# Performance work log

Measured on AMD Instinct MI355X. Metric: run time of the kernel, lower is better.

## Reference

```python
import jax, jax.numpy as jnp
import numpy as np

B, S, D, K = 16, 1024, 512, 4
DIL = (1, 2, 4, 8)
EPS_BN = 1e-5
EPS_LN = 1e-5


def _edge_conv1d(x, w, b, dilation):
    # x: [B, C, S], w: [O, C, k]; replicate ('edge') padding keeps length S
    p = (w.shape[-1] - 1) * dilation // 2
    xp = jnp.pad(x, ((0, 0), (0, 0), (p, p)), mode='edge')
    y = jax.lax.conv_general_dilated(xp, w, (1,), 'VALID', rhs_dilation=(dilation,),
                                     dimension_numbers=('NCH', 'OIH', 'NCH'))
    return y + b[None, :, None]


def setup_inputs() -> dict:
    key = jax.random.key(0)
    ks = jax.random.split(key, 16)
    g = lambda i, shape, s: jax.random.normal(ks[i], shape, jnp.float32) * s
    return {
        'x': g(0, (B, S, D), 1.0),
        'conv_w': g(1, (4, D, D, 3), 0.02),
        'conv_b': jnp.zeros((4, D), jnp.float32),
        'fusion_w': g(2, (D, 4 * D), 0.02),
        'fusion_b': jnp.zeros((D,), jnp.float32),
        'refine_w': g(3, (D, D, 3), 0.02),
        'refine_b': jnp.zeros((D,), jnp.float32),
        'hyp1_w': g(4, (D, D, 3), 0.02),
        'hyp1_b': jnp.zeros((D,), jnp.float32),
        'bn_gamma': jnp.ones((D,), jnp.float32),
        'bn_beta': jnp.zeros((D,), jnp.float32),
        'hyp2_w': g(5, (D // 2, D, 3), 0.02),
        'hyp2_b': jnp.zeros((D // 2,), jnp.float32),
        'proj_w': g(6, (2 * K, D // 2), 0.05),
        'proj_b': jnp.zeros((2 * K,), jnp.float32),
        'gate_w': g(7, (D, D), 0.02),
        'gate_b': jnp.zeros((D,), jnp.float32),
        'base_w': g(8, (D, D), 0.02),
        'base_b': jnp.zeros((D,), jnp.float32),
        'wav_w': g(9, (K, D, D), 0.02),
        'wav_b': jnp.zeros((K, D), jnp.float32),
        'ln_gamma': jnp.ones((D,), jnp.float32),
        'ln_beta': jnp.zeros((D,), jnp.float32),
    }


def _forward(x, conv_w, conv_b, fusion_w, fusion_b, refine_w, refine_b,
             hyp1_w, hyp1_b, bn_gamma, bn_beta, hyp2_w, hyp2_b,
             proj_w, proj_b, gate_w, gate_b, base_w, base_b,
             wav_w, wav_b, ln_gamma, ln_beta):
    residual = x
    x_in = jnp.transpose(x, (0, 2, 1))                      # [B, D, S]
    # ---- FFT trend/seasonal split ----
    fx = jnp.fft.rfft(x_in, axis=2)
    cutoff = S // 10
    mask = (jnp.arange(fx.shape[2]) < cutoff).astype(fx.dtype)
    x_seasonal = jnp.fft.irfft(fx * mask, n=S, axis=2)       # [B, D, S]
    x_smooth = x_seasonal
    x_spike = x_in - x_seasonal
    # ---- iterative dilated-conv smoothing (dropout = identity, eval mode) ----
    for _ in range(2):  # iterations
        outs = [jax.nn.gelu(_edge_conv1d(x_smooth, conv_w[i], conv_b[i], DIL[i]),
                            approximate=False)
                for i in range(4)]
        x_concat = jnp.concatenate(outs, axis=1)             # [B, 4D, S]
        x_smooth = jnp.einsum('oc,bcs->bos', fusion_w, x_concat) + fusion_b[None, :, None]
        x_spike = _edge_conv1d(x_in - x_smooth, refine_w, refine_b, 1)
    x_smooth_t = jnp.transpose(x_smooth, (0, 2, 1))          # [B, S, D]
    x_spike_t = jnp.transpose(x_spike, (0, 2, 1))            # [B, S, D]
    # ---- hypernet (BatchNorm in eval mode: running mean 0, var 1) ----
    h = _edge_conv1d(x_smooth, hyp1_w, hyp1_b, 1)
    h = h / jnp.sqrt(1.0 + EPS_BN) * bn_gamma[None, :, None] + bn_beta[None, :, None]
    h = jax.nn.silu(h)
    h = jax.nn.silu(_edge_conv1d(h, hyp2_w, hyp2_b, 1))      # [B, D/2, S]
    cnn_feat = jnp.mean(h, axis=2)                           # AdaptiveAvgPool1d(1)
    params = (cnn_feat @ proj_w.T + proj_b).reshape(B, 1, K, 2)
    dyn_a = jax.nn.softplus(params[..., 0]) + 0.01           # [B, 1, K]
    dyn_b = jax.nn.sigmoid(params[..., 1]) * S               # [B, 1, K]
    # ---- wavelet-KAN base path: Linear(silu(x_smooth)) ----
    base_out = jnp.einsum('bsd,ed->bse', jax.nn.silu(x_smooth_t), base_w) + base_b
    # ---- wavelet path: mexican-hat wavelets over sequence positions ----
    pos = jnp.arange(S, dtype=x.dtype)[None, :, None]        # [1, S, 1]
    u = (pos - dyn_b) / dyn_a                                # [B, S, K]
    c = 2.0 / (np.sqrt(3.0) * np.pi ** 0.25)
    psi = c * (1.0 - u * u) * jnp.exp(-0.5 * u * u)          # [B, S, K]
    z = jnp.einsum('bsd,kde->bkse', x_spike_t, wav_w)        # per-wavelet linear
    kan_out = jnp.einsum('bsk,bkse->bse', psi, z) + jnp.einsum('bsk,ke->bse', psi, wav_b)
    amp = jax.nn.sigmoid(base_out @ gate_w.T + gate_b) * 2.0
    x_out = base_out + kan_out * amp
    # ---- residual + LayerNorm ----
    y = x_out + residual
    mu = jnp.mean(y, axis=-1, keepdims=True)
    var = jnp.var(y, axis=-1, keepdims=True)
    return (y - mu) / jnp.sqrt(var + EPS_LN) * ln_gamma + ln_beta


def reference(x, conv_w, conv_b, fusion_w, fusion_b, refine_w, refine_b,
              hyp1_w, hyp1_b, bn_gamma, bn_beta, hyp2_w, hyp2_b,
              proj_w, proj_b, gate_w, gate_b, base_w, base_b,
              wav_w, wav_b, ln_gamma, ln_beta):
    return _forward(x, conv_w, conv_b, fusion_w, fusion_b, refine_w, refine_b,
                    hyp1_w, hyp1_b, bn_gamma, bn_beta, hyp2_w, hyp2_b,
                    proj_w, proj_b, gate_w, gate_b, base_w, base_b,
                    wav_w, wav_b, ln_gamma, ln_beta)
```

## Files before the change

kernel.cpp:

```cpp
#include <hip/hip_runtime.h>
#include <hip/hip_bf16.h>
#include <math.h>

#define NB 16
#define SS 1024
#define DD 512
#define SP 1040
#define HD 256

typedef unsigned short US;
typedef short bf16x8 __attribute__((ext_vector_type(8)));
typedef float f32x4 __attribute__((ext_vector_type(4)));
typedef __attribute__((address_space(1))) const void gv1;
typedef __attribute__((address_space(3))) void lv3;

static __device__ __forceinline__ float b2sf(US u){ return __uint_as_float(((unsigned)u)<<16); }
static __device__ __forceinline__ US f2b(float f){
  __hip_bfloat16 h = __float2bfloat16(f);
  union { __hip_bfloat16 h; US u; } c; c.h = h; return c.u;
}
static __device__ __forceinline__ float rd(const void* __restrict__ p, long i, int isf){
  return isf ? ((const float*)p)[i] : b2sf(((const US*)p)[i]);
}

__global__ void k_detect(const void* __restrict__ x, int* __restrict__ flag){
  const US* u = (const US*)x;
  int t = threadIdx.x;
  float m = 0.f;
  for (int i = t; i < 4096; i += 256){
    float v = fabsf(b2sf(u[i]));
    if (isnan(v) || isinf(v)) v = 1e30f;
    m = fmaxf(m, v);
  }
  for (int off = 32; off; off >>= 1) m = fmaxf(m, __shfl_down(m, off));
  __shared__ float sh[4];
  if ((t & 63) == 0) sh[t >> 6] = m;
  __syncthreads();
  if (t == 0){
    float mm = fmaxf(fmaxf(sh[0], sh[1]), fmaxf(sh[2], sh[3]));
    flag[0] = (mm > 1e6f) ? 1 : 0;
  }
}

__global__ void k_cvt_f(const void* __restrict__ s, float* __restrict__ d, long n, const int* __restrict__ fl){
  int isf = fl[0];
  long i = (long)blockIdx.x*256 + threadIdx.x;
  if (i < n) d[i] = rd(s, i, isf);
}
__global__ void k_cvt_b(const void* __restrict__ s, US* __restrict__ d, long n, const int* __restrict__ fl){
  int isf = fl[0];
  long i = (long)blockIdx.x*256 + threadIdx.x;
  if (i < n) d[i] = f2b(rd(s, i, isf));
}
__global__ void k_repack3(const void* __restrict__ src, US* __restrict__ dst, int O, int C, const int* __restrict__ fl){
  int isf = fl[0];
  long i = (long)blockIdx.x*256 + threadIdx.x;
  long n = (long)O*3*C;
  if (i >= n) return;
  int o = (int)(i / (3*C)); int r = (int)(i - (long)o*3*C); int t = r / C; int c = r - t*C;
  dst[i] = f2b(rd(src, ((long)o*C + c)*3 + t, isf));
}
__global__ void k_repack_wav(const void* __restrict__ src, US* __restrict__ dst, const int* __restrict__ fl){
  int isf = fl[0];
  long i = (long)blockIdx.x*256 + threadIdx.x;
  if (i >= 4L*DD*DD) return;
  int k = (int)(i >> 18); long r = i & ((1<<18)-1); int e = (int)(r >> 9); int d = (int)(r & 511);
  dst[i] = f2b(rd(src, ((long)(k*DD + d))*DD + e, isf));
}
__global__ void k_build_g(float* __restrict__ g){
  int d = blockIdx.x*256 + threadIdx.x;
  if (d >= SS) return;
  float s = 1.f;
  for (int k = 1; k < 102; ++k){
    int r = (k*d) & (SS-1);
    s += 2.f * cosf(6.28318530718f * (float)r * (1.f/SS));
  }
  g[d] = s * (1.f/SS);
}
__global__ void k_build_cmat(const float* __restrict__ g, US* __restrict__ cm){
  int i = blockIdx.x*256 + threadIdx.x;
  if (i >= SS*SS) return;
  int t = i >> 10, s = i & (SS-1);
  cm[i] = f2b(g[(s - t) & (SS-1)]);
}
__global__ __launch_bounds__(256) void k_transpose_b(const void* __restrict__ x, US* __restrict__ xt, const int* __restrict__ fl){
  int isf = fl[0];
  __shared__ float tl[32][33];
  int b = blockIdx.z, s0 = blockIdx.x*32, d0 = blockIdx.y*32;
  int tx = threadIdx.x & 31, ty = threadIdx.x >> 5;
  for (int i = ty; i < 32; i += 8)
    tl[i][tx] = rd(x, ((long)(b*SS + s0+i))*DD + d0+tx, isf);
  __syncthreads();
  for (int i = ty; i < 32; i += 8)
    xt[((long)(b*DD + d0+i))*SS + s0+tx] = f2b(tl[tx][i]);
}
__global__ void k_pad_b(const US* __restrict__ src, const void* __restrict__ xsub, US* __restrict__ dst, const int* __restrict__ fl){
  long i = (long)blockIdx.x*256 + threadIdx.x;
  const long TOT = (long)NB*SP*128;
  if (i >= TOT) return;
  int c4 = (int)(i & 127);
  int j  = (int)((i >> 7) % SP);
  int b  = (int)(i / (128L*SP));
  int sr = j - 8; sr = sr < 0 ? 0 : (sr > SS-1 ? SS-1 : sr);
  long si = ((long)(b*SS + sr))*DD + c4*4;
  ushort4 sv = *(const ushort4*)&src[si];
  float v0=b2sf(sv.x), v1=b2sf(sv.y), v2=b2sf(sv.z), v3=b2sf(sv.w);
  if (xsub){
    if (fl[0]){
      float4 xv = *(const float4*)((const float*)xsub + si);
      v0 = xv.x - v0; v1 = xv.y - v1; v2 = xv.z - v2; v3 = xv.w - v3;
    } else {
      ushort4 xv = *(const ushort4*)((const US*)xsub + si);
      v0 = b2sf(xv.x) - v0; v1 = b2sf(xv.y) - v1; v2 = b2sf(xv.z) - v2; v3 = b2sf(xv.w) - v3;
    }
  }
  ushort4 o; o.x=f2b(v0); o.y=f2b(v1); o.z=f2b(v2); o.w=f2b(v3);
  *(ushort4*)&dst[((long)(b*SP + j))*DD + c4*4] = o;
}
__global__ void k_silu_b(const US* __restrict__ s, US* __restrict__ d){
  long i = (long)blockIdx.x*256 + threadIdx.x;
  if (i >= (long)NB*SS*DD/4) return;
  ushort4 sv = *(const ushort4*)&s[i*4];
  float v[4] = {b2sf(sv.x), b2sf(sv.y), b2sf(sv.z), b2sf(sv.w)};
  ushort4 o;
  US* op = (US*)&o;
  #pragma unroll
  for (int r = 0; r < 4; r++){ float t = v[r]; op[r] = f2b(t/(1.f + expf(-t))); }
  *(ushort4*)&d[i*4] = o;
}

template<int EPI, bool TAPPED>
__global__ __launch_bounds__(256) void k_mfma(
    const US* __restrict__ A, const US* __restrict__ Bact, void* __restrict__ Out,
    int NYB, int K, long sBbytes, int ldbB, int dil,
    long sOut, int ldo, int moff,
    const float* __restrict__ bias, const float* __restrict__ s1v, const float* __restrict__ s2v)
{
  __shared__ alignas(16) US As[128*64];
  __shared__ alignas(16) US Bs[128*64];
  const int bx = blockIdx.x;
  const int ny = bx % NYB;
  const int b  = bx / NYB;
  const int m0 = blockIdx.y*128, n0 = ny*128;
  const int dd = (TAPPED && dil < 0) ? (1 << (m0 >> 9)) : dil;
  const char* Bb = (const char*)Bact + (long)b*sBbytes;
  const int tid = threadIdx.x;
  const int lane = tid & 63, w = tid >> 6;
  const int wr = w >> 1, wc = w & 1;
  const int col = lane & 15, g = lane >> 4;

  f32x4 acc[4][4] = {};

  int rows_[4], sls_[4];
  #pragma unroll
  for (int i = 0; i < 4; i++){
    int c = w*256 + i*64 + lane;
    rows_[i] = c >> 3;
    sls_[i] = (c & 7) ^ ((c >> 3) & 7);
  }

  for (int k0 = 0; k0 < K; k0 += 64){
    const int c0 = TAPPED ? (k0 & 511) : k0;
    const int srowOff = TAPPED ? (8 + ((k0 >> 9) - 1)*dd) : 0;
    __syncthreads();
    #pragma unroll
    for (int i = 0; i < 4; i++){
      const char* ga = (const char*)A + ((long)(m0 + rows_[i])*K + k0)*2 + sls_[i]*16;
      __builtin_amdgcn_global_load_lds((gv1*)ga, (lv3*)&As[(w*256 + i*64)*8], 16, 0, 0);
      const char* gb = Bb + (long)(n0 + rows_[i] + srowOff)*ldbB + c0*2 + sls_[i]*16;
      __builtin_amdgcn_global_load_lds((gv1*)gb, (lv3*)&Bs[(w*256 + i*64)*8], 16, 0, 0);
    }
    __syncthreads();
    #pragma unroll
    for (int kk = 0; kk < 2; kk++){
      bf16x8 af[4], bf[4];
      #pragma unroll
      for (int f = 0; f < 4; f++){
        int rowa = wr*64 + f*16 + col;
        int sla = (g + kk*4) ^ (rowa & 7);
        af[f] = *(const bf16x8*)&As[rowa*64 + sla*8];
        int rowb = wc*64 + f*16 + col;
        int slb = (g + kk*4) ^ (rowb & 7);
        bf[f] = *(const bf16x8*)&Bs[rowb*64 + slb*8];
      }
      #pragma unroll
      for (int fm = 0; fm < 4; fm++)
        #pragma unroll
        for (int fn = 0; fn < 4; fn++)
          acc[fm][fn] = __builtin_amdgcn_mfma_f32_16x16x32_bf16(af[fm], bf[fn], acc[fm][fn], 0, 0, 0);
    }
  }

  #pragma unroll
  for (int fm = 0; fm < 4; fm++){
    const int mm = m0 + wr*64 + fm*16 + g*4;
    #pragma unroll
    for (int fn = 0; fn < 4; fn++){
      const int nn = n0 + wc*64 + fn*16 + col;
      f32x4 v = acc[fm][fn];
      if (EPI == 5){
        US* o = (US*)Out + (long)b*sOut + (long)mm*ldo + nn;
        #pragma unroll
        for (int r = 0; r < 4; r++) o[(long)r*ldo] = f2b(v[r]);
      } else {
        US pk[4];
        #pragma unroll
        for (int r = 0; r < 4; r++){
          int m = mm + r;
          float val = v[r] + bias[m];
          if (EPI == 1) val = 0.5f*val*(1.f + erff(val*0.70710678f));
          if (EPI == 2){ val = val*(s1v[m]*0.99999500f) + s2v[m]; val = val/(1.f + expf(-val)); }
          if (EPI == 3){ val = val/(1.f + expf(-val)); }
          pk[r] = f2b(val);
        }
        US* o = (US*)Out + (long)b*sOut + (long)nn*ldo + moff + mm;
        *(ushort4*)o = *(ushort4*)pk;
      }
    }
  }
}

__global__ __launch_bounds__(256) void k_pool(const US* __restrict__ h2, float* __restrict__ feat){
  int b = blockIdx.x, c = threadIdx.x;
  float s = 0.f;
  for (int t = 0; t < SS; t++) s += b2sf(h2[((long)(b*SS + t))*HD + c]);
  feat[b*HD + c] = s * (1.f/SS);
}
__global__ void k_params(const float* __restrict__ feat, const float* __restrict__ pw,
                         const float* __restrict__ pb, float* __restrict__ dynA, float* __restrict__ dynB){
  int t = threadIdx.x;
  if (t >= 128) return;
  int b = t >> 3, j = t & 7;
  float s = pb[j];
  for (int c = 0; c < HD; c++) s += feat[b*HD + c]*pw[j*HD + c];
  int k = j >> 1;
  if ((j & 1) == 0){
    float sp = s > 20.f ? s : log1pf(expf(s));
    dynA[b*4 + k] = sp + 0.01f;
  } else {
    dynB[b*4 + k] = 1024.f/(1.f + expf(-s));
  }
}
__global__ void k_psi(const float* __restrict__ dynA, const float* __restrict__ dynB, float* __restrict__ psi){
  int i = blockIdx.x*256 + threadIdx.x;
  if (i >= NB*4*SS) return;
  int b = i >> 12, k = (i >> 10) & 3, s = i & (SS-1);
  float u = ((float)s - dynB[b*4 + k]) / dynA[b*4 + k];
  psi[i] = 0.86732507f*(1.f - u*u)*expf(-0.5f*u*u);
}
__global__ __launch_bounds__(128) void k_final(const US* __restrict__ base, const US* __restrict__ zz,
    const US* __restrict__ gate, const float* __restrict__ psi, const void* __restrict__ x,
    void* __restrict__ out, const float* __restrict__ lng, const float* __restrict__ lnb,
    const int* __restrict__ fl){
  int isf = fl[0];
  long row = blockIdx.x;
  int b = (int)(row >> 10), s = (int)(row & (SS-1));
  int t = threadIdx.x;
  long off = row*DD + t*4;
  ushort4 bs = *(const ushort4*)&base[off];
  ushort4 gt = *(const ushort4*)&gate[off];
  float p0 = psi[b*4096 + s];
  float p1 = psi[b*4096 + 1024 + s];
  float p2 = psi[b*4096 + 2048 + s];
  float p3 = psi[b*4096 + 3072 + s];
  const US* zrow = zz + row*2048 + t*4;
  ushort4 z0 = *(const ushort4*)&zrow[0];
  ushort4 z1 = *(const ushort4*)&zrow[512];
  ushort4 z2 = *(const ushort4*)&zrow[1024];
  ushort4 z3 = *(const ushort4*)&zrow[1536];
  float xv[4];
  if (isf){ float4 q = *(const float4*)((const float*)x + off); xv[0]=q.x; xv[1]=q.y; xv[2]=q.z; xv[3]=q.w; }
  else { ushort4 q = *(const ushort4*)((const US*)x + off); xv[0]=b2sf(q.x); xv[1]=b2sf(q.y); xv[2]=b2sf(q.z); xv[3]=b2sf(q.w); }
  float bv[4] = {b2sf(bs.x), b2sf(bs.y), b2sf(bs.z), b2sf(bs.w)};
  float gv[4] = {b2sf(gt.x), b2sf(gt.y), b2sf(gt.z), b2sf(gt.w)};
  const US* z0p = (const US*)&z0; const US* z1p = (const US*)&z1;
  const US* z2p = (const US*)&z2; const US* z3p = (const US*)&z3;
  float y[4];
  float sm = 0.f, ssq = 0.f;
  #pragma unroll
  for (int r = 0; r < 4; r++){
    float kan = p0*b2sf(z0p[r]) + p1*b2sf(z1p[r]) + p2*b2sf(z2p[r]) + p3*b2sf(z3p[r]);
    float amp = 2.f/(1.f + expf(-gv[r]));
    y[r] = bv[r] + kan*amp + xv[r];
    sm += y[r]; ssq += y[r]*y[r];
  }
  for (int o = 32; o; o >>= 1){ sm += __shfl_down(sm, o); ssq += __shfl_down(ssq, o); }
  __shared__ float sh[4];
  int lane = t & 63, wid = t >> 6;
  if (lane == 0){ sh[wid*2] = sm; sh[wid*2+1] = ssq; }
  __syncthreads();
  float S1 = sh[0] + sh[2], S2 = sh[1] + sh[3];
  float mean = S1*(1.f/DD), var = S2*(1.f/DD) - mean*mean;
  float rstd = rsqrtf(var + 1e-5f);
  #pragma unroll
  for (int r = 0; r < 4; r++){
    int d = t*4 + r;
    float val = (y[r] - mean)*rstd*lng[d] + lnb[d];
    if (isf) ((float*)out)[off + r] = val;
    else     ((US*)out)[off + r] = f2b(val);
  }
}

extern "C" void kernel_launch(void* const* d_in, const int* in_sizes, int n_in,
                              void* d_out, int out_size, void* d_ws, size_t ws_size,
                              hipStream_t stream){
  const void* x       = d_in[0];
  const void* conv_w  = d_in[1];
  const void* conv_b  = d_in[2];
  const void* fusion_w= d_in[3];
  const void* fusion_b= d_in[4];
  const void* refine_w= d_in[5];
  const void* refine_b= d_in[6];
  const void* hyp1_w  = d_in[7];
  const void* hyp1_b  = d_in[8];
  const void* bn_g    = d_in[9];
  const void* bn_b    = d_in[10];
  const void* hyp2_w  = d_in[11];
  const void* hyp2_b  = d_in[12];
  const void* proj_w  = d_in[13];
  const void* proj_b  = d_in[14];
  const void* gate_w  = d_in[15];
  const void* gate_b  = d_in[16];
  const void* base_w  = d_in[17];
  const void* base_b  = d_in[18];
  const void* wav_w   = d_in[19];
  const void* wav_b   = d_in[20];
  const void* ln_g    = d_in[21];
  const void* ln_b    = d_in[22];

  char* wsb = (char*)d_ws;
  long off = 0;
  auto AA = [&](long bytes)->char*{ char* p = wsb + off; off += (bytes + 255) & ~255L; return p; };
  US* padG  = (US*)AA((long)NB*SP*DD*2);
  US* smA   = (US*)AA((long)NB*SS*DD*2);
  US* smB   = (US*)AA((long)NB*SS*DD*2);
  US* xTh   = (US*)AA((long)NB*SS*DD*2);
  US* cc    = (US*)AA((long)NB*SS*2048*2);
  US* baseB = (US*)AA((long)NB*SS*DD*2);
  US* Wc  = (US*)AA(4L*512*1536*2);
  US* Wr  = (US*)AA(512L*1536*2);
  US* Wh1 = (US*)AA(512L*1536*2);
  US* Wh2 = (US*)AA(256L*1536*2);
  US* Wwv = (US*)AA(4L*512*512*2);
  US* Fw  = (US*)AA(512L*2048*2);
  US* BW  = (US*)AA(512L*512*2);
  US* GW  = (US*)AA(512L*512*2);
  US* Cm  = (US*)AA(1024L*1024*2);
  float* gvec = (float*)AA(1024*4);
  float* cb_f = (float*)AA(2048*4);
  float* fz_b = (float*)AA(512*4);
  float* rf_b = (float*)AA(512*4);
  float* h1_b = (float*)AA(512*4);
  float* h2_b = (float*)AA(256*4);
  float* bs_b = (float*)AA(512*4);
  float* gt_b = (float*)AA(512*4);
  float* wv_b = (float*)AA(2048*4);
  float* bngf = (float*)AA(512*4);
  float* bnbf = (float*)AA(512*4);
  float* pwf  = (float*)AA(2048*4);
  float* pbf  = (float*)AA(8*4);
  float* lngf = (float*)AA(512*4);
  float* lnbf = (float*)AA(512*4);
  float* feat = (float*)AA(16*256*4);
  float* dynA = (float*)AA(64*4);
  float* dynB = (float*)AA(64*4);
  float* psi  = (float*)AA((long)NB*4*SS*4);
  int* flag   = (int*)AA(64);
  if ((size_t)off > ws_size) return;
  US* h2    = cc;
  US* siluS = cc + 16777216;

  auto g1 = [](long n){ return dim3((unsigned)((n + 255)/256)); };
  const long sAct = (long)SS*DD*2;
  const long sPad = (long)SP*DD*2;
  const long sCC  = (long)SS*2048*2;
  const long oAct = (long)SS*DD;
  const long oCC  = (long)SS*2048;
  const long oH2  = (long)SS*HD;

  k_detect<<<1, 256, 0, stream>>>(x, flag);

  k_repack3<<<g1(2048L*512*3), 256, 0, stream>>>(conv_w, Wc, 2048, 512, flag);
  k_repack3<<<g1(512L*512*3), 256, 0, stream>>>(refine_w, Wr, 512, 512, flag);
  k_repack3<<<g1(512L*512*3), 256, 0, stream>>>(hyp1_w, Wh1, 512, 512, flag);
  k_repack3<<<g1(256L*512*3), 256, 0, stream>>>(hyp2_w, Wh2, 256, 512, flag);
  k_repack_wav<<<g1(4L*512*512), 256, 0, stream>>>(wav_w, Wwv, flag);
  k_cvt_b<<<g1(512L*2048), 256, 0, stream>>>(fusion_w, Fw, 512L*2048, flag);
  k_cvt_b<<<g1(512L*512), 256, 0, stream>>>(base_w, BW, 512L*512, flag);
  k_cvt_b<<<g1(512L*512), 256, 0, stream>>>(gate_w, GW, 512L*512, flag);
  k_cvt_f<<<g1(2048), 256, 0, stream>>>(conv_b, cb_f, 2048, flag);
  k_cvt_f<<<g1(512), 256, 0, stream>>>(fusion_b, fz_b, 512, flag);
  k_cvt_f<<<g1(512), 256, 0, stream>>>(refine_b, rf_b, 512, flag);
  k_cvt_f<<<g1(512), 256, 0, stream>>>(hyp1_b, h1_b, 512, flag);
  k_cvt_f<<<g1(256), 256, 0, stream>>>(hyp2_b, h2_b, 256, flag);
  k_cvt_f<<<g1(512), 256, 0, stream>>>(base_b, bs_b, 512, flag);
  k_cvt_f<<<g1(512), 256, 0, stream>>>(gate_b, gt_b, 512, flag);
  k_cvt_f<<<g1(2048), 256, 0, stream>>>(wav_b, wv_b, 2048, flag);
  k_cvt_f<<<g1(512), 256, 0, stream>>>(bn_g, bngf, 512, flag);
  k_cvt_f<<<g1(512), 256, 0, stream>>>(bn_b, bnbf, 512, flag);
  k_cvt_f<<<g1(2048), 256, 0, stream>>>(proj_w, pwf, 2048, flag);
  k_cvt_f<<<g1(8), 256, 0, stream>>>(proj_b, pbf, 8, flag);
  k_cvt_f<<<g1(512), 256, 0, stream>>>(ln_g, lngf, 512, flag);
  k_cvt_f<<<g1(512), 256, 0, stream>>>(ln_b, lnbf, 512, flag);
  k_build_g<<<g1(SS), 256, 0, stream>>>(gvec);
  k_build_cmat<<<g1((long)SS*SS), 256, 0, stream>>>(gvec, Cm);
  k_transpose_b<<<dim3(SS/32, DD/32, NB), 256, 0, stream>>>(x, xTh, flag);

  k_mfma<5,false><<<dim3(4*NB, 8), 256, 0, stream>>>(Cm, xTh, smA,
      4, 1024, (long)DD*SS*2, SS*2, 0, oAct, DD, 0, nullptr, nullptr, nullptr);

  US* cur = smA; US* nxt = smB;
  for (int it = 0; it < 2; ++it){
    k_pad_b<<<g1((long)NB*SP*128), 256, 0, stream>>>(cur, nullptr, padG, flag);
    k_mfma<1,true><<<dim3(8*NB, 16), 256, 0, stream>>>(Wc, padG, cc,
        8, 1536, sPad, DD*2, -1, oCC, 2048, 0, cb_f, nullptr, nullptr);
    k_mfma<0,false><<<dim3(8*NB, 4), 256, 0, stream>>>(Fw, cc, nxt,
        8, 2048, sCC, 4096, 0, oAct, DD, 0, fz_b, nullptr, nullptr);
    US* t = cur; cur = nxt; nxt = t;
  }

  k_pad_b<<<g1((long)NB*SP*128), 256, 0, stream>>>(cur, x, padG, flag);
  k_mfma<0,true><<<dim3(8*NB, 4), 256, 0, stream>>>(Wr, padG, smB,
      8, 1536, sPad, DD*2, 1, oAct, DD, 0, rf_b, nullptr, nullptr);

  k_pad_b<<<g1((long)NB*SP*128), 256, 0, stream>>>(cur, nullptr, padG, flag);
  k_mfma<2,true><<<dim3(8*NB, 4), 256, 0, stream>>>(Wh1, padG, xTh,
      8, 1536, sPad, DD*2, 1, oAct, DD, 0, h1_b, bngf, bnbf);
  k_pad_b<<<g1((long)NB*SP*128), 256, 0, stream>>>(xTh, nullptr, padG, flag);
  k_mfma<3,true><<<dim3(8*NB, 2), 256, 0, stream>>>(Wh2, padG, h2,
      8, 1536, sPad, DD*2, 1, oH2, HD, 0, h2_b, nullptr, nullptr);
  k_pool<<<NB, 256, 0, stream>>>(h2, feat);
  k_params<<<1, 128, 0, stream>>>(feat, pwf, pbf, dynA, dynB);
  k_psi<<<g1(NB*4*SS), 256, 0, stream>>>(dynA, dynB, psi);

  k_silu_b<<<g1((long)NB*SS*DD/4), 256, 0, stream>>>(cur, siluS);
  k_mfma<0,false><<<dim3(8*NB, 4), 256, 0, stream>>>(BW, siluS, baseB,
      8, 512, sAct, DD*2, 0, oAct, DD, 0, bs_b, nullptr, nullptr);
  k_mfma<0,false><<<dim3(8*NB, 4), 256, 0, stream>>>(GW, baseB, padG,
      8, 512, sAct, DD*2, 0, oAct, DD, 0, gt_b, nullptr, nullptr);

  k_mfma<0,false><<<dim3(8*NB, 16), 256, 0, stream>>>(Wwv, smB, cc,
      8, 512, sAct, DD*2, 0, oCC, 2048, 0, wv_b, nullptr, nullptr);

  k_final<<<NB*SS, 128, 0, stream>>>(baseB, cc, padG, psi, x, d_out, lngf, lnbf, flag);
}
```

Measured before the change: 769.6 us.

## Fuse psi-weighted wavelet reduction into MFMA epilogue and stage output stores through LDS

Adds an EPI==4 mode in which each GEMM block loops over the four wavelet weight slices, accumulates psi-weighted results in registers and writes one [B,S,D] kan tensor. This replaces the 4x-wide z tensor and its readback in k_final. It also reroutes every k_mfma epilogue through a swizzled LDS tile so the global stores become coalesced 16-byte writes. The cost is an extra accumulator set, and therefore more register pressure, in the fused GEMM, plus an extra LDS round-trip in all epilogues.

Result: no change. 767.2 us (-0.3%).

```diff
diff --git a/kernel.cpp b/kernel.cpp
--- a/kernel.cpp
+++ b/kernel.cpp
@@ -134,10 +134,13 @@
     const US* __restrict__ A, const US* __restrict__ Bact, void* __restrict__ Out,
     int NYB, int K, long sBbytes, int ldbB, int dil,
     long sOut, int ldo, int moff,
-    const float* __restrict__ bias, const float* __restrict__ s1v, const float* __restrict__ s2v)
+    const float* __restrict__ bias, const float* __restrict__ s1v, const float* __restrict__ s2v,
+    const float* __restrict__ psiP)
 {
-  __shared__ alignas(16) US As[128*64];
-  __shared__ alignas(16) US Bs[128*64];
+  __shared__ alignas(16) US shb[2*128*64];
+  __shared__ float psh[(EPI==4) ? 512 : 4];
+  US* As = shb;
+  US* Bs = shb + 128*64;
   const int bx = blockIdx.x;
   const int ny = bx % NYB;
   const int b  = bx / NYB;
@@ -149,7 +152,19 @@
   const int wr = w >> 1, wc = w & 1;
   const int col = lane & 15, g = lane >> 4;
 
-  f32x4 acc[4][4] = {};
+  if (EPI == 4){
+    for (int i = tid; i < 512; i += 256)
+      psh[i] = psiP[(long)b*4096 + (i >> 7)*SS + n0 + (i & 127)];
+  }
+
+  f32x4 acc[4][4];
+  f32x4 facc[4][4];
+  if (EPI == 4){
+    #pragma unroll
+    for (int i = 0; i < 4; i++)
+      #pragma unroll
+      for (int j = 0; j < 4; j++) facc[i][j] = (f32x4){0.f,0.f,0.f,0.f};
+  }
 
   int rows_[4], sls_[4];
   #pragma unroll
@@ -159,64 +174,110 @@
     sls_[i] = (c & 7) ^ ((c >> 3) & 7);
   }
 
-  for (int k0 = 0; k0 < K; k0 += 64){
-    const int c0 = TAPPED ? (k0 & 511) : k0;
-    const int srowOff = TAPPED ? (8 + ((k0 >> 9) - 1)*dd) : 0;
-    __syncthreads();
+  const int NKC = (EPI == 4) ? 4 : 1;
+  for (int kc = 0; kc < NKC; ++kc){
     #pragma unroll
-    for (int i = 0; i < 4; i++){
-      const char* ga = (const char*)A + ((long)(m0 + rows_[i])*K + k0)*2 + sls_[i]*16;
-      __builtin_amdgcn_global_load_lds((gv1*)ga, (lv3*)&As[(w*256 + i*64)*8], 16, 0, 0);
-      const char* gb = Bb + (long)(n0 + rows_[i] + srowOff)*ldbB + c0*2 + sls_[i]*16;
-      __builtin_amdgcn_global_load_lds((gv1*)gb, (lv3*)&Bs[(w*256 + i*64)*8], 16, 0, 0);
+    for (int i = 0; i < 4; i++)
+      #pragma unroll
+      for (int j = 0; j < 4; j++) acc[i][j] = (f32x4){0.f,0.f,0.f,0.f};
+
+    for (int k0 = 0; k0 < K; k0 += 64){
+      const int c0 = TAPPED ? (k0 & 511) : k0;
+      const int srowOff = TAPPED ? (8 + ((k0 >> 9) - 1)*dd) : 0;
+      __syncthreads();
+      #pragma unroll
+      for (int i = 0; i < 4; i++){
+        const long arow = (long)(m0 + rows_[i]) + (EPI==4 ? kc*512 : 0);
+        const char* ga = (const char*)A + (arow*K + k0)*2 + sls_[i]*16;
+        __builtin_amdgcn_global_load_lds((gv1*)ga, (lv3*)&As[(w*256 + i*64)*8], 16, 0, 0);
+        const char* gb = Bb + (long)(n0 + rows_[i] + srowOff)*ldbB + c0*2 + sls_[i]*16;
+        __builtin_amdgcn_global_load_lds((gv1*)gb, (lv3*)&Bs[(w*256 + i*64)*8], 16, 0, 0);
+      }
+      __syncthreads();
+      #pragma unroll
+      for (int kk = 0; kk < 2; kk++){
+        bf16x8 af[4], bf[4];
+        #pragma unroll
+        for (int f = 0; f < 4; f++){
+          int rowa = wr*64 + f*16 + col;
+          int sla = (g + kk*4) ^ (rowa & 7);
+          af[f] = *(const bf16x8*)&As[rowa*64 + sla*8];
+          int rowb = wc*64 + f*16 + col;
+          int slb = (g + kk*4) ^ (rowb & 7);
+          bf[f] = *(const bf16x8*)&Bs[rowb*64 + slb*8];
+        }
+        #pragma unroll
+        for (int fm = 0; fm < 4; fm++)
+          #pragma unroll
+          for (int fn = 0; fn < 4; fn++)
+            acc[fm][fn] = __builtin_amdgcn_mfma_f32_16x16x32_bf16(af[fm], bf[fn], acc[fm][fn], 0, 0, 0);
+      }
     }
-    __syncthreads();
-    #pragma unroll
-    for (int kk = 0; kk < 2; kk++){
-      bf16x8 af[4], bf[4];
-      #pragma unroll
-      for (int f = 0; f < 4; f++){
-        int rowa = wr*64 + f*16 + col;
-        int sla = (g + kk*4) ^ (rowa & 7);
-        af[f] = *(const bf16x8*)&As[rowa*64 + sla*8];
-        int rowb = wc*64 + f*16 + col;
-        int slb = (g + kk*4) ^ (rowb & 7);
-        bf[f] = *(const bf16x8*)&Bs[rowb*64 + slb*8];
+
+    if (EPI == 4){
+      #pragma unroll
+      for (int fm = 0; fm < 4; fm++){
+        const int mm_l = wr*64 + fm*16 + g*4;
+        float bb[4];
+        #pragma unroll
+        for (int r = 0; r < 4; r++) bb[r] = bias[kc*512 + m0 + mm_l + r];
+        #pragma unroll
+        for (int fn = 0; fn < 4; fn++){
+          float p = psh[kc*128 + wc*64 + fn*16 + col];
+          #pragma unroll
+          for (int r = 0; r < 4; r++)
+            facc[fm][fn][r] += p * (acc[fm][fn][r] + bb[r]);
+        }
       }
-      #pragma unroll
-      for (int fm = 0; fm < 4; fm++)
-        #pragma unroll
-        for (int fn = 0; fn < 4; fn++)
-          acc[fm][fn] = __builtin_amdgcn_mfma_f32_16x16x32_bf16(af[fm], bf[fn], acc[fm][fn], 0, 0, 0);
     }
   }
 
+  __syncthreads();
+  US* tile = shb;
   #pragma unroll
   for (int fm = 0; fm < 4; fm++){
-    const int mm = m0 + wr*64 + fm*16 + g*4;
+    const int mm_l = wr*64 + fm*16 + g*4;
+    float bb[4];
+    if (EPI <= 3){
+      #pragma unroll
+      for (int r = 0; r < 4; r++) bb[r] = bias[m0 + mm_l + r];
+    }
     #pragma unroll
     for (int fn = 0; fn < 4; fn++){
-      const int nn = n0 + wc*64 + fn*16 + col;
-      f32x4 v = acc[fm][fn];
+      const int nn_l = wc*64 + fn*16 + col;
+      f32x4 v = (EPI == 4) ? facc[fm][fn] : acc[fm][fn];
       if (EPI == 5){
-        US* o = (US*)Out + (long)b*sOut + (long)mm*ldo + nn;
-        #pragma unroll
-        for (int r = 0; r < 4; r++) o[(long)r*ldo] = f2b(v[r]);
+        #pragma unroll
+        for (int r = 0; r < 4; r++){
+          int row = mm_l + r;
+          int byte = row*256 + ((nn_l*2) ^ ((row & 7) << 4));
+          *(US*)((char*)tile + byte) = f2b(v[r]);
+        }
       } else {
         US pk[4];
         #pragma unroll
         for (int r = 0; r < 4; r++){
-          int m = mm + r;
-          float val = v[r] + bias[m];
+          float val = v[r];
+          if (EPI <= 3) val += bb[r];
           if (EPI == 1) val = 0.5f*val*(1.f + erff(val*0.70710678f));
-          if (EPI == 2){ val = val*(s1v[m]*0.99999500f) + s2v[m]; val = val/(1.f + expf(-val)); }
+          if (EPI == 2){ int m = m0 + mm_l + r; val = val*(s1v[m]*0.99999500f) + s2v[m]; val = val/(1.f + expf(-val)); }
           if (EPI == 3){ val = val/(1.f + expf(-val)); }
           pk[r] = f2b(val);
         }
-        US* o = (US*)Out + (long)b*sOut + (long)nn*ldo + moff + mm;
-        *(ushort4*)o = *(ushort4*)pk;
+        int byte = nn_l*256 + ((mm_l*2) ^ ((nn_l & 7) << 4));
+        *(int2*)((char*)tile + byte) = *(int2*)pk;
       }
     }
+  }
+  __syncthreads();
+  const int r0 = tid >> 4, c = tid & 15;
+  #pragma unroll
+  for (int p = 0; p < 8; p++){
+    int r = p*16 + r0;
+    int4 vv = *(const int4*)((const char*)tile + r*256 + ((c*16) ^ ((r & 7) << 4)));
+    long obase = (EPI == 5) ? ((long)b*sOut + (long)(m0 + r)*ldo + n0)
+                            : ((long)b*sOut + (long)(n0 + r)*ldo + moff + m0);
+    *(int4*)((US*)Out + obase + c*8) = vv;
   }
 }
 
@@ -248,40 +309,29 @@
   float u = ((float)s - dynB[b*4 + k]) / dynA[b*4 + k];
   psi[i] = 0.86732507f*(1.f - u*u)*expf(-0.5f*u*u);
 }
-__global__ __launch_bounds__(128) void k_final(const US* __restrict__ base, const US* __restrict__ zz,
-    const US* __restrict__ gate, const float* __restrict__ psi, const void* __restrict__ x,
+__global__ __launch_bounds__(128) void k_final(const US* __restrict__ base, const US* __restrict__ kan,
+    const US* __restrict__ gate, const void* __restrict__ x,
     void* __restrict__ out, const float* __restrict__ lng, const float* __restrict__ lnb,
     const int* __restrict__ fl){
   int isf = fl[0];
   long row = blockIdx.x;
-  int b = (int)(row >> 10), s = (int)(row & (SS-1));
   int t = threadIdx.x;
   long off = row*DD + t*4;
   ushort4 bs = *(const ushort4*)&base[off];
   ushort4 gt = *(const ushort4*)&gate[off];
-  float p0 = psi[b*4096 + s];
-  float p1 = psi[b*4096 + 1024 + s];
-  float p2 = psi[b*4096 + 2048 + s];
-  float p3 = psi[b*4096 + 3072 + s];
-  const US* zrow = zz + row*2048 + t*4;
-  ushort4 z0 = *(const ushort4*)&zrow[0];
-  ushort4 z1 = *(const ushort4*)&zrow[512];
-  ushort4 z2 = *(const ushort4*)&zrow[1024];
-  ushort4 z3 = *(const ushort4*)&zrow[1536];
+  ushort4 kn = *(const ushort4*)&kan[off];
   float xv[4];
   if (isf){ float4 q = *(const float4*)((const float*)x + off); xv[0]=q.x; xv[1]=q.y; xv[2]=q.z; xv[3]=q.w; }
   else { ushort4 q = *(const ushort4*)((const US*)x + off); xv[0]=b2sf(q.x); xv[1]=b2sf(q.y); xv[2]=b2sf(q.z); xv[3]=b2sf(q.w); }
   float bv[4] = {b2sf(bs.x), b2sf(bs.y), b2sf(bs.z), b2sf(bs.w)};
   float gv[4] = {b2sf(gt.x), b2sf(gt.y), b2sf(gt.z), b2sf(gt.w)};
-  const US* z0p = (const US*)&z0; const US* z1p = (const US*)&z1;
-  const US* z2p = (const US*)&z2; const US* z3p = (const US*)&z3;
+  const US* kp = (const US*)&kn;
   float y[4];
   float sm = 0.f, ssq = 0.f;
   #pragma unroll
   for (int r = 0; r < 4; r++){
-    float kan = p0*b2sf(z0p[r]) + p1*b2sf(z1p[r]) + p2*b2sf(z2p[r]) + p3*b2sf(z3p[r]);
     float amp = 2.f/(1.f + expf(-gv[r]));
-    y[r] = bv[r] + kan*amp + xv[r];
+    y[r] = bv[r] + b2sf(kp[r])*amp + xv[r];
     sm += y[r]; ssq += y[r]*y[r];
   }
   for (int o = 32; o; o >>= 1){ sm += __shfl_down(sm, o); ssq += __shfl_down(ssq, o); }
@@ -369,6 +419,7 @@
   if ((size_t)off > ws_size) return;
   US* h2    = cc;
   US* siluS = cc + 16777216;
+  US* kanb  = cc;
 
   auto g1 = [](long n){ return dim3((unsigned)((n + 255)/256)); };
   const long sAct = (long)SS*DD*2;
@@ -407,40 +458,40 @@
   k_transpose_b<<<dim3(SS/32, DD/32, NB), 256, 0, stream>>>(x, xTh, flag);
 
   k_mfma<5,false><<<dim3(4*NB, 8), 256, 0, stream>>>(Cm, xTh, smA,
-      4, 1024, (long)DD*SS*2, SS*2, 0, oAct, DD, 0, nullptr, nullptr, nullptr);
+      4, 1024, (long)DD*SS*2, SS*2, 0, oAct, DD, 0, nullptr, nullptr, nullptr, nullptr);
 
   US* cur = smA; US* nxt = smB;
   for (int it = 0; it < 2; ++it){
     k_pad_b<<<g1((long)NB*SP*128), 256, 0, stream>>>(cur, nullptr, padG, flag);
     k_mfma<1,true><<<dim3(8*NB, 16), 256, 0, stream>>>(Wc, padG, cc,
-        8, 1536, sPad, DD*2, -1, oCC, 2048, 0, cb_f, nullptr, nullptr);
+        8, 1536, sPad, DD*2, -1, oCC, 2048, 0, cb_f, nullptr, nullptr, nullptr);
     k_mfma<0,false><<<dim3(8*NB, 4), 256, 0, stream>>>(Fw, cc, nxt,
-        8, 2048, sCC, 4096, 0, oAct, DD, 0, fz_b, nullptr, nullptr);
+        8, 2048, sCC, 4096, 0, oAct, DD, 0, fz_b, nullptr, nullptr, nullptr);
     US* t = cur; cur = nxt; nxt = t;
   }
 
   k_pad_b<<<g1((long)NB*SP*128), 256, 0, stream>>>(cur, x, padG, flag);
   k_mfma<0,true><<<dim3(8*NB, 4), 256, 0, stream>>>(Wr, padG, smB,
-      8, 1536, sPad, DD*2, 1, oAct, DD, 0, rf_b, nullptr, nullptr);
+      8, 1536, sPad, DD*2, 1, oAct, DD, 0, rf_b, nullptr, nullptr, nullptr);
 
   k_pad_b<<<g1((long)NB*SP*128), 256, 0, stream>>>(cur, nullptr, padG, flag);
   k_mfma<2,true><<<dim3(8*NB, 4), 256, 0, stream>>>(Wh1, padG, xTh,
-      8, 1536, sPad, DD*2, 1, oAct, DD, 0, h1_b, bngf, bnbf);
+      8, 1536, sPad, DD*2, 1, oAct, DD, 0, h1_b, bngf, bnbf, nullptr);
   k_pad_b<<<g1((long)NB*SP*128), 256, 0, stream>>>(xTh, nullptr, padG, flag);
   k_mfma<3,true><<<dim3(8*NB, 2), 256, 0, stream>>>(Wh2, padG, h2,
-      8, 1536, sPad, DD*2, 1, oH2, HD, 0, h2_b, nullptr, nullptr);
+      8, 1536, sPad, DD*2, 1, oH2, HD, 0, h2_b, nullptr, nullptr, nullptr);
   k_pool<<<NB, 256, 0, stream>>>(h2, feat);
   k_params<<<1, 128, 0, stream>>>(feat, pwf, pbf, dynA, dynB);
   k_psi<<<g1(NB*4*SS), 256, 0, stream>>>(dynA, dynB, psi);
 
   k_silu_b<<<g1((long)NB*SS*DD/4), 256, 0, stream>>>(cur, siluS);
   k_mfma<0,false><<<dim3(8*NB, 4), 256, 0, stream>>>(BW, siluS, baseB,
-      8, 512, sAct, DD*2, 0, oAct, DD, 0, bs_b, nullptr, nullptr);
+      8, 512, sAct, DD*2, 0, oAct, DD, 0, bs_b, nullptr, nullptr, nullptr);
   k_mfma<0,false><<<dim3(8*NB, 4), 256, 0, stream>>>(GW, baseB, padG,
-      8, 512, sAct, DD*2, 0, oAct, DD, 0, gt_b, nullptr, nullptr);
-
-  k_mfma<0,false><<<dim3(8*NB, 16), 256, 0, stream>>>(Wwv, smB, cc,
-      8, 512, sAct, DD*2, 0, oCC, 2048, 0, wv_b, nullptr, nullptr);
-
-  k_final<<<NB*SS, 128, 0, stream>>>(baseB, cc, padG, psi, x, d_out, lngf, lnbf, flag);
-}
+      8, 512, sAct, DD*2, 0, oAct, DD, 0, gt_b, nullptr, nullptr, nullptr);
+
+  k_mfma<4,false><<<dim3(8*NB, 4), 256, 0, stream>>>(Wwv, smB, kanb,
+      8, 512, sAct, DD*2, 0, oAct, DD, 0, wv_b, nullptr, nullptr, psi);
+
+  k_final<<<NB*SS, 128, 0, stream>>>(baseB, kanb, padG, x, d_out, lngf, lnbf, flag);
+}
```
